# Optimization experiments

Hardware: AMD Instinct MI355X
Metric: run time of the kernel (lower is better)

Reference implementation:

```python
import jax, jax.numpy as jnp
import numpy as np

N = 100000      # nodes (single node type)
E = 400000      # edges per relation
R = 4           # relations
DIN = 128       # h_dim
H1 = 8          # heads, layer 1
DH1 = DIN // H1 # per-head dim, layer 1
DOUT = 128      # out_dim (layer 2 has 1 head of dim DOUT)
NEG_SLOPE = 0.2 # GATConv default leaky_relu slope


def gat_rel_layer(h, src, dst, W, al, ar, loop_w, bias, activation):
    """One RelationalAttLayer: per-relation GATConv (bias=False), summed across
    relations, + self-loop matmul + bias + optional relu. dropout=0.
    h: [N, din]; src/dst: [R, E]; W: [R, din, H*Dh]; al/ar: [R, H, Dh];
    loop_w: [din, dout]; bias: [dout]."""
    n = h.shape[0]

    def per_rel(src_r, dst_r, W_r, al_r, ar_r):
        nh, dh = al_r.shape
        Wh = (h @ W_r).reshape(n, nh, dh)                 # [N,H,Dh]
        el = jnp.sum(Wh * al_r, axis=-1)                  # [N,H]
        er = jnp.sum(Wh * ar_r, axis=-1)                  # [N,H]
        e = jax.nn.leaky_relu(el[src_r] + er[dst_r], NEG_SLOPE)  # [E,H]
        # edge-softmax over incoming edges per destination node (stable)
        m = jax.lax.stop_gradient(jax.ops.segment_max(e, dst_r, num_segments=n))
        ex = jnp.exp(e - m[dst_r])
        denom = jax.ops.segment_sum(ex, dst_r, num_segments=n)  # [N,H]
        alpha = ex / denom[dst_r]                                # [E,H]
        # scatter-aggregate messages
        return jax.ops.segment_sum(alpha[:, :, None] * Wh[src_r], dst_r,
                                   num_segments=n)               # [N,H,Dh]

    outs = jax.vmap(per_rel)(src, dst, W, al, ar)  # [R,N,H,Dh]
    hout = outs.sum(0).reshape(n, -1)              # cross-relation sum, flatten heads
    hout = hout + h @ loop_w + bias                # self-loop + h_bias
    if activation:
        hout = jax.nn.relu(hout)
    return hout


def setup_inputs() -> dict:
    key = jax.random.key(0)
    ks = jax.random.split(key, 14)
    s = 0.1
    return {
        "h": jax.random.normal(ks[0], (N, DIN), dtype=jnp.float32),
        "src_idx": jax.random.randint(ks[1], (R, E), 0, N, dtype=jnp.int32),
        "dst_idx": jax.random.randint(ks[2], (R, E), 0, N, dtype=jnp.int32),
        # layer 1 params (h_dim -> h_dim, H1 heads)
        "W1": jax.random.normal(ks[3], (R, DIN, H1 * DH1), dtype=jnp.float32) * s,
        "al1": jax.random.normal(ks[4], (R, H1, DH1), dtype=jnp.float32) * s,
        "ar1": jax.random.normal(ks[5], (R, H1, DH1), dtype=jnp.float32) * s,
        "loop1": jax.random.normal(ks[6], (DIN, DIN), dtype=jnp.float32) * s,
        "b1": jnp.zeros((DIN,), dtype=jnp.float32),
        # layer 2 params (h_dim -> out_dim, 1 head)
        "W2": jax.random.normal(ks[7], (R, DIN, DOUT), dtype=jnp.float32) * s,
        "al2": jax.random.normal(ks[8], (R, 1, DOUT), dtype=jnp.float32) * s,
        "ar2": jax.random.normal(ks[9], (R, 1, DOUT), dtype=jnp.float32) * s,
        "loop2": jax.random.normal(ks[10], (DIN, DOUT), dtype=jnp.float32) * s,
        "b2": jnp.zeros((DOUT,), dtype=jnp.float32),
    }


def reference(h, src_idx, dst_idx, W1, al1, ar1, loop1, b1,
              W2, al2, ar2, loop2, b2):
    # hidden layer: relu activation; last layer: no activation (last_layer_act=False)
    h1 = gat_rel_layer(h, src_idx, dst_idx, W1, al1, ar1, loop1, b1, activation=True)
    h2 = gat_rel_layer(h1, src_idx, dst_idx, W2, al2, ar2, loop2, b2, activation=False)
    return h2
```

## Files before the change

### kernel.cpp

```cpp
#include <hip/hip_runtime.h>

#define NN 100000
#define NE 400000
#define NREL 4
#define MAXDEG 24

typedef unsigned short u16;
typedef __attribute__((ext_vector_type(8))) short bf16x8;
typedef __attribute__((ext_vector_type(4))) float f32x4;

__device__ __forceinline__ u16 f2bf(float x) {
    union { float f; unsigned int u; } v; v.f = x;
    unsigned int r = v.u + 0x7fffu + ((v.u >> 16) & 1u);
    return (u16)(r >> 16);
}
__device__ __forceinline__ float bf2f(u16 x) {
    union { unsigned int u; float f; } v; v.u = ((unsigned int)x) << 16;
    return v.f;
}

__global__ __launch_bounds__(256) void zero_cnt_kernel(int* __restrict__ cnt, int n)
{
    int i = blockIdx.x * 256 + threadIdx.x;
    if (i < n) cnt[i] = 0;
}

template <bool RELU>
__global__ __launch_bounds__(256) void conv_kernel(
    const float* __restrict__ X, u16* __restrict__ Xb, int n8)
{
    int i = blockIdx.x * 256 + threadIdx.x;
    if (i >= n8) return;
    float4 a = ((const float4*)X)[2 * i];
    float4 b = ((const float4*)X)[2 * i + 1];
    if (RELU) {
        a.x = fmaxf(a.x, 0.f); a.y = fmaxf(a.y, 0.f);
        a.z = fmaxf(a.z, 0.f); a.w = fmaxf(a.w, 0.f);
        b.x = fmaxf(b.x, 0.f); b.y = fmaxf(b.y, 0.f);
        b.z = fmaxf(b.z, 0.f); b.w = fmaxf(b.w, 0.f);
    }
    ushort4 lo, hi;
    lo.x = f2bf(a.x); lo.y = f2bf(a.y); lo.z = f2bf(a.z); lo.w = f2bf(a.w);
    hi.x = f2bf(b.x); hi.y = f2bf(b.y); hi.z = f2bf(b.z); hi.w = f2bf(b.w);
    ((ushort4*)Xb)[2 * i] = lo;
    ((ushort4*)Xb)[2 * i + 1] = hi;
}

__global__ __launch_bounds__(256) void build_bcat_kernel(
    const float* __restrict__ W, const float* __restrict__ loopw,
    u16* __restrict__ Bcat)
{
    int id = blockIdx.x * 256 + threadIdx.x;
    if (id >= 5 * 16384) return;
    int slot = id >> 14, rem = id & 16383;
    int c = rem >> 7, k = rem & 127;
    const float* M = (slot < 4) ? (W + slot * 16384) : loopw;
    Bcat[(size_t)c * 640 + slot * 128 + k] = f2bf(M[k * 128 + c]);
}

__global__ __launch_bounds__(256) void build_w_kernel(
    const float* __restrict__ W, const float* __restrict__ al,
    const float* __restrict__ ar, u16* __restrict__ wcatB, int nh, int dh)
{
    int id = blockIdx.x * 256 + threadIdx.x;
    if (id >= 16384) return;
    int j = id >> 7, k = id & 127;
    int P2 = 8 * nh;
    float s = 0.f;
    if (j < P2) {
        int half = 4 * nh;
        int jj = (j < half) ? j : j - half;
        const float* av = (j < half) ? al : ar;
        int r = jj / nh, hh = jj % nh;
        for (int i = 0; i < dh; ++i)
            s += W[r * 16384 + k * 128 + hh * dh + i] * av[(r * nh + hh) * dh + i];
    }
    wcatB[j * 128 + k] = f2bf(s);
}

__global__ __launch_bounds__(256) void csr_build_kernel(
    const int* __restrict__ src, const int* __restrict__ dst,
    int* __restrict__ cur, int* __restrict__ bucket)
{
    int i = blockIdx.x * 256 + threadIdx.x;
    if (i >= NE) return;
    int d0 = dst[i],          s0 = src[i];
    int d1 = dst[NE + i],     s1 = src[NE + i];
    int d2 = dst[2 * NE + i], s2 = src[2 * NE + i];
    int d3 = dst[3 * NE + i], s3 = src[3 * NE + i];
    int p0 = atomicAdd(&cur[d0], 1);
    int p1 = atomicAdd(&cur[NN + d1], 1);
    int p2 = atomicAdd(&cur[2 * NN + d2], 1);
    int p3 = atomicAdd(&cur[3 * NN + d3], 1);
    if (p0 < MAXDEG) bucket[(size_t)d0 * MAXDEG + p0] = s0;
    if (p1 < MAXDEG) bucket[((size_t)NN + d1) * MAXDEG + p1] = s1;
    if (p2 < MAXDEG) bucket[((size_t)2 * NN + d2) * MAXDEG + p2] = s2;
    if (p3 < MAXDEG) bucket[((size_t)3 * NN + d3) * MAXDEG + p3] = s3;
}

__global__ __launch_bounds__(256) void fused_gemm_kernel(
    const u16* __restrict__ Xb, const u16* __restrict__ Bcat,
    const u16* __restrict__ wcatB, u16* __restrict__ Wh,
    float* __restrict__ O, const float* __restrict__ bias,
    float* __restrict__ elrR, int n)
{
    __shared__ u16 sA[64][136];
    __shared__ u16 sB[128][136];
    const int tid = threadIdx.x;
    const int y = blockIdx.y;
    const int row0 = blockIdx.x * 64;
    const u16* bbase; int bstride;
    if (y < 5) { bbase = Bcat + y * 128; bstride = 640; }
    else       { bbase = wcatB;          bstride = 128; }

#pragma unroll
    for (int i = 0; i < 8; ++i) {
        int idx = tid + 256 * i;
        int r = idx >> 4, ch = idx & 15;
        *(float4*)&sB[r][ch * 8] = *(const float4*)(bbase + (size_t)r * bstride + ch * 8);
    }
#pragma unroll
    for (int i = 0; i < 4; ++i) {
        int idx = tid + 256 * i;
        int r = idx >> 4, ch = idx & 15;
        int gr = row0 + r;
        float4 v = make_float4(0.f, 0.f, 0.f, 0.f);
        if (gr < n) v = *(const float4*)(Xb + (size_t)gr * 128 + ch * 8);
        *(float4*)&sA[r][ch * 8] = v;
    }
    __syncthreads();

    const int w = tid >> 6, lane = tid & 63;
    const int lr = lane & 15, hi = lane >> 4;
    f32x4 acc[8];
#pragma unroll
    for (int fn = 0; fn < 8; ++fn) acc[fn] = (f32x4){0.f, 0.f, 0.f, 0.f};
#pragma unroll
    for (int ko = 0; ko < 4; ++ko) {
        const int kk = ko * 32 + hi * 8;
        bf16x8 a = *(const bf16x8*)&sA[w * 16 + lr][kk];
#pragma unroll
        for (int fn = 0; fn < 8; ++fn) {
            bf16x8 b = *(const bf16x8*)&sB[fn * 16 + lr][kk];
            acc[fn] = __builtin_amdgcn_mfma_f32_16x16x32_bf16(a, b, acc[fn], 0, 0, 0);
        }
    }

    if (y < 4) {
        u16* Wr = Wh + (size_t)y * NN * 128;
#pragma unroll
        for (int reg = 0; reg < 4; ++reg) {
            int grow = row0 + w * 16 + hi * 4 + reg;
            if (grow >= n) continue;
            u16* crow = Wr + (size_t)grow * 128;
#pragma unroll
            for (int fn = 0; fn < 8; ++fn)
                crow[fn * 16 + lr] = f2bf(acc[fn][reg]);
        }
    } else if (y == 4) {
#pragma unroll
        for (int reg = 0; reg < 4; ++reg) {
            int grow = row0 + w * 16 + hi * 4 + reg;
            if (grow >= n) continue;
            float* crow = O + (size_t)grow * 128;
#pragma unroll
            for (int fn = 0; fn < 8; ++fn) {
                int col = fn * 16 + lr;
                crow[col] = acc[fn][reg] + bias[col];
            }
        }
    } else {
#pragma unroll
        for (int reg = 0; reg < 4; ++reg) {
            int grow = row0 + w * 16 + hi * 4 + reg;
            if (grow >= n) continue;
#pragma unroll
            for (int fn = 0; fn < 8; ++fn) {
                int col = fn * 16 + lr;
                if (col < 64) {
                    int jj  = (col < 32) ? col : col - 32;
                    int r   = jj >> 3, hh = jj & 7;
                    int off = (col < 32) ? hh : 8 + hh;
                    elrR[((size_t)r * NN + grow) * 16 + off] = acc[fn][reg];
                }
            }
        }
    }
}

__global__ __launch_bounds__(256) void elr2_gemm_kernel(
    const u16* __restrict__ Xb, const u16* __restrict__ wcatB,
    float* __restrict__ elrR, int n)
{
    __shared__ u16 sA[64][136];
    __shared__ u16 sB[16][136];
    const int tid = threadIdx.x;
    const int row0 = blockIdx.x * 64;

    if (tid < 256) {
        int r = tid >> 4, ch = tid & 15;
        *(float4*)&sB[r][ch * 8] = *(const float4*)(wcatB + (size_t)r * 128 + ch * 8);
    }
#pragma unroll
    for (int i = 0; i < 4; ++i) {
        int idx = tid + 256 * i;
        int r = idx >> 4, ch = idx & 15;
        int gr = row0 + r;
        float4 v = make_float4(0.f, 0.f, 0.f, 0.f);
        if (gr < n) v = *(const float4*)(Xb + (size_t)gr * 128 + ch * 8);
        *(float4*)&sA[r][ch * 8] = v;
    }
    __syncthreads();

    const int w = tid >> 6, lane = tid & 63;
    const int lr = lane & 15, hi = lane >> 4;
    f32x4 acc = (f32x4){0.f, 0.f, 0.f, 0.f};
#pragma unroll
    for (int ko = 0; ko < 4; ++ko) {
        const int kk = ko * 32 + hi * 8;
        bf16x8 a = *(const bf16x8*)&sA[w * 16 + lr][kk];
        bf16x8 b = *(const bf16x8*)&sB[lr][kk];
        acc = __builtin_amdgcn_mfma_f32_16x16x32_bf16(a, b, acc, 0, 0, 0);
    }
#pragma unroll
    for (int reg = 0; reg < 4; ++reg) {
        int grow = row0 + w * 16 + hi * 4 + reg;
        if (grow >= n) continue;
        int col = lr;
        if (col < 8) {
            int r = (col < 4) ? col : col - 4;
            int off = (col < 4) ? 0 : 1;
            elrR[((size_t)r * NN + grow) * 2 + off] = acc[reg];
        }
    }
}

__global__ __launch_bounds__(256) void gather_rel_kernel(
    const int* __restrict__ cnt, const int* __restrict__ bucket,
    const float* __restrict__ elP, const u16* __restrict__ WhR,
    float* __restrict__ O)
{
    const int d = blockIdx.x * 4 + (threadIdx.x >> 6);
    if (d >= NN) return;
    const int lane = threadIdx.x & 63;
    const int c0 = lane * 2;
    const int hh = c0 >> 4;

    int deg = cnt[d];
    deg = deg < 0 ? 0 : (deg > MAXDEG ? MAXDEG : deg);
    const int* bk = bucket + (size_t)d * MAXDEG;
    int4 q0 = make_int4(0, 0, 0, 0), q1 = make_int4(0, 0, 0, 0);
    if (deg > 0) q0 = *(const int4*)bk;
    if (deg > 4) q1 = *(const int4*)(bk + 4);
    const float erd = elP[(size_t)d * 16 + 8 + hh];

    float dn = 0.f, m0 = 0.f, m1 = 0.f;
    const int ss[8] = {q0.x, q0.y, q0.z, q0.w, q1.x, q1.y, q1.z, q1.w};
#pragma unroll
    for (int e = 0; e < 8; ++e) {
        int s = ss[e];
        s = ((unsigned)s < (unsigned)NN) ? s : 0;
        float v = elP[(size_t)s * 16 + hh] + erd;
        ushort2 wv = *(const ushort2*)(WhR + (size_t)s * 128 + c0);
        v = v > 0.f ? v : 0.2f * v;
        float ex = (e < deg) ? __expf(v) : 0.f;
        dn += ex;
        m0 = fmaf(ex, bf2f(wv.x), m0);
        m1 = fmaf(ex, bf2f(wv.y), m1);
    }
    for (int e = 8; e < deg; ++e) {
        int s = bk[e];
        s = ((unsigned)s < (unsigned)NN) ? s : 0;
        float v = elP[(size_t)s * 16 + hh] + erd;
        v = v > 0.f ? v : 0.2f * v;
        float ex = __expf(v);
        ushort2 wv = *(const ushort2*)(WhR + (size_t)s * 128 + c0);
        dn += ex;
        m0 = fmaf(ex, bf2f(wv.x), m0);
        m1 = fmaf(ex, bf2f(wv.y), m1);
    }
    float inv = (deg > 0) ? 1.f / dn : 0.f;
    float2* op = (float2*)(O + (size_t)d * 128) + lane;
    float2 c = *op;
    c.x += m0 * inv;
    c.y += m1 * inv;
    *op = c;
}

__global__ __launch_bounds__(256) void gather_x_kernel(
    const int* __restrict__ cnt, const int* __restrict__ bucket,
    const float* __restrict__ elrR, const u16* __restrict__ Xb,
    u16* __restrict__ Xagg)
{
    const int d = blockIdx.x;
    const int w = threadIdx.x >> 6;
    const int lane = threadIdx.x & 63;
    const int c0 = lane * 2;

    int deg = cnt[w * NN + d];
    deg = deg < 0 ? 0 : (deg > MAXDEG ? MAXDEG : deg);
    const int* bk = bucket + ((size_t)w * NN + d) * MAXDEG;
    int4 q0 = make_int4(0, 0, 0, 0), q1 = make_int4(0, 0, 0, 0);
    if (deg > 0) q0 = *(const int4*)bk;
    if (deg > 4) q1 = *(const int4*)(bk + 4);
    const float* elP = elrR + (size_t)w * NN * 2;
    const float erd = elP[(size_t)d * 2 + 1];

    float dn = 0.f, m0 = 0.f, m1 = 0.f;
    const int ss[8] = {q0.x, q0.y, q0.z, q0.w, q1.x, q1.y, q1.z, q1.w};
#pragma unroll
    for (int e = 0; e < 8; ++e) {
        int s = ss[e];
        s = ((unsigned)s < (unsigned)NN) ? s : 0;
        float v = elP[(size_t)s * 2] + erd;
        ushort2 wv = *(const ushort2*)(Xb + (size_t)s * 128 + c0);
        v = v > 0.f ? v : 0.2f * v;
        float ex = (e < deg) ? __expf(v) : 0.f;
        dn += ex;
        m0 = fmaf(ex, bf2f(wv.x), m0);
        m1 = fmaf(ex, bf2f(wv.y), m1);
    }
    for (int e = 8; e < deg; ++e) {
        int s = bk[e];
        s = ((unsigned)s < (unsigned)NN) ? s : 0;
        float v = elP[(size_t)s * 2] + erd;
        v = v > 0.f ? v : 0.2f * v;
        float ex = __expf(v);
        ushort2 wv = *(const ushort2*)(Xb + (size_t)s * 128 + c0);
        dn += ex;
        m0 = fmaf(ex, bf2f(wv.x), m0);
        m1 = fmaf(ex, bf2f(wv.y), m1);
    }
    float inv = (deg > 0) ? 1.f / dn : 0.f;
    u16* orow = Xagg + ((size_t)w * NN + d) * 128;
    ushort2 o;
    o.x = f2bf(m0 * inv);
    o.y = f2bf(m1 * inv);
    *(ushort2*)(orow + c0) = o;
}

__global__ __launch_bounds__(256) void big_gemm_kernel(
    const u16* __restrict__ Xagg, const u16* __restrict__ Xb,
    const u16* __restrict__ Bcat, const float* __restrict__ bias,
    float* __restrict__ out, int n)
{
    __shared__ u16 sA[64][136];
    __shared__ u16 sB[128][136];
    const int tid = threadIdx.x;
    const int row0 = blockIdx.x * 64;
    const int w = tid >> 6, lane = tid & 63;
    const int lr = lane & 15, hi = lane >> 4;

    f32x4 acc[8];
#pragma unroll
    for (int fn = 0; fn < 8; ++fn) acc[fn] = (f32x4){0.f, 0.f, 0.f, 0.f};

    for (int kc = 0; kc < 5; ++kc) {
        const u16* Amat = (kc < 4) ? (Xagg + (size_t)kc * NN * 128) : Xb;
        if (kc) __syncthreads();
#pragma unroll
        for (int i = 0; i < 8; ++i) {
            int idx = tid + 256 * i;
            int r = idx >> 4, ch = idx & 15;
            *(float4*)&sB[r][ch * 8] =
                *(const float4*)(Bcat + (size_t)r * 640 + kc * 128 + ch * 8);
        }
#pragma unroll
        for (int i = 0; i < 4; ++i) {
            int idx = tid + 256 * i;
            int r = idx >> 4, ch = idx & 15;
            int gr = row0 + r;
            float4 v = make_float4(0.f, 0.f, 0.f, 0.f);
            if (gr < n) v = *(const float4*)(Amat + (size_t)gr * 128 + ch * 8);
            *(float4*)&sA[r][ch * 8] = v;
        }
        __syncthreads();
#pragma unroll
        for (int ko = 0; ko < 4; ++ko) {
            const int kk = ko * 32 + hi * 8;
            bf16x8 a = *(const bf16x8*)&sA[w * 16 + lr][kk];
#pragma unroll
            for (int fn = 0; fn < 8; ++fn) {
                bf16x8 b = *(const bf16x8*)&sB[fn * 16 + lr][kk];
                acc[fn] = __builtin_amdgcn_mfma_f32_16x16x32_bf16(a, b, acc[fn], 0, 0, 0);
            }
        }
    }

#pragma unroll
    for (int reg = 0; reg < 4; ++reg) {
        int grow = row0 + w * 16 + hi * 4 + reg;
        if (grow >= n) continue;
        float* crow = out + (size_t)grow * 128;
#pragma unroll
        for (int fn = 0; fn < 8; ++fn) {
            int col = fn * 16 + lr;
            crow[col] = acc[fn][reg] + bias[col];
        }
    }
}

extern "C" void kernel_launch(void* const* d_in, const int* in_sizes, int n_in,
                              void* d_out, int out_size, void* d_ws, size_t ws_size,
                              hipStream_t stream)
{
    const float* h   = (const float*)d_in[0];
    const int*   src = (const int*)d_in[1];
    const int*   dst = (const int*)d_in[2];
    const float* W1  = (const float*)d_in[3];
    const float* al1 = (const float*)d_in[4];
    const float* ar1 = (const float*)d_in[5];
    const float* lp1 = (const float*)d_in[6];
    const float* b1  = (const float*)d_in[7];
    const float* W2  = (const float*)d_in[8];
    const float* al2 = (const float*)d_in[9];
    const float* ar2 = (const float*)d_in[10];
    const float* lp2 = (const float*)d_in[11];
    const float* b2  = (const float*)d_in[12];

    float* out = (float*)d_out;
    char*  p   = (char*)d_ws;

    const size_t szXb   = (size_t)NN * 128 * 2;
    const size_t szO    = (size_t)NN * 128 * 4;
    const size_t szElr  = (size_t)NREL * NN * 16 * 4;
    const size_t szCnt  = (size_t)NREL * NN * 4;
    const size_t szBkt  = (size_t)NREL * NN * MAXDEG * 4;
    const size_t szBcat = 5 * 16384 * 2;
    const size_t szWc   = 16384 * 2;

    u16*   Xb     = (u16*)p;    p += szXb;
    float* O1     = (float*)p;  p += szO;
    float* elrR   = (float*)p;  p += szElr;
    int*   cnt    = (int*)p;    p += szCnt;
    int*   bucket = (int*)p;    p += szBkt;
    u16*   Bcat   = (u16*)p;    p += szBcat;
    u16*   wcatB  = (u16*)p;    p += szWc;
    u16*   Wh     = (u16*)p;

    const int gg = (NN + 63) / 64;
    const int n8 = NN * 128 / 8;

    zero_cnt_kernel<<<(NREL * NN + 255) / 256, 256, 0, stream>>>(cnt, NREL * NN);
    csr_build_kernel<<<(NE + 255) / 256, 256, 0, stream>>>(src, dst, cnt, bucket);
    conv_kernel<false><<<(n8 + 255) / 256, 256, 0, stream>>>(h, Xb, n8);

    build_bcat_kernel<<<(5 * 16384) / 256, 256, 0, stream>>>(W1, lp1, Bcat);
    build_w_kernel<<<16384 / 256, 256, 0, stream>>>(W1, al1, ar1, wcatB, 8, 16);
    fused_gemm_kernel<<<dim3(gg, 6), 256, 0, stream>>>(
        Xb, Bcat, wcatB, Wh, O1, b1, elrR, NN);
    for (int r = 0; r < NREL; ++r)
        gather_rel_kernel<<<(NN + 3) / 4, 256, 0, stream>>>(
            cnt + (size_t)r * NN, bucket + (size_t)r * NN * MAXDEG,
            elrR + (size_t)r * NN * 16, Wh + (size_t)r * NN * 128, O1);
    conv_kernel<true><<<(n8 + 255) / 256, 256, 0, stream>>>(O1, Xb, n8);

    build_bcat_kernel<<<(5 * 16384) / 256, 256, 0, stream>>>(W2, lp2, Bcat);
    build_w_kernel<<<16384 / 256, 256, 0, stream>>>(W2, al2, ar2, wcatB, 1, 128);
    elr2_gemm_kernel<<<gg, 256, 0, stream>>>(Xb, wcatB, elrR, NN);
    gather_x_kernel<<<NN, 256, 0, stream>>>(cnt, bucket, elrR, Xb, Wh);
    big_gemm_kernel<<<gg, 256, 0, stream>>>(Wh, Xb, Bcat, b2, out, NN);
}
```

Measured before the change: 789.7 us.

## Fuse layer-1 relation gathers with ReLU/bf16 conversion; enlarge GEMM row tiles

```diff
diff --git a/kernel.cpp b/kernel.cpp
--- a/kernel.cpp
+++ b/kernel.cpp
@@ -25,7 +25,6 @@
     if (i < n) cnt[i] = 0;
 }
 
-template <bool RELU>
 __global__ __launch_bounds__(256) void conv_kernel(
     const float* __restrict__ X, u16* __restrict__ Xb, int n8)
 {
@@ -33,12 +32,6 @@
     if (i >= n8) return;
     float4 a = ((const float4*)X)[2 * i];
     float4 b = ((const float4*)X)[2 * i + 1];
-    if (RELU) {
-        a.x = fmaxf(a.x, 0.f); a.y = fmaxf(a.y, 0.f);
-        a.z = fmaxf(a.z, 0.f); a.w = fmaxf(a.w, 0.f);
-        b.x = fmaxf(b.x, 0.f); b.y = fmaxf(b.y, 0.f);
-        b.z = fmaxf(b.z, 0.f); b.w = fmaxf(b.w, 0.f);
-    }
     ushort4 lo, hi;
     lo.x = f2bf(a.x); lo.y = f2bf(a.y); lo.z = f2bf(a.z); lo.w = f2bf(a.w);
     hi.x = f2bf(b.x); hi.y = f2bf(b.y); hi.z = f2bf(b.z); hi.w = f2bf(b.w);
@@ -104,11 +97,11 @@
     float* __restrict__ O, const float* __restrict__ bias,
     float* __restrict__ elrR, int n)
 {
-    __shared__ u16 sA[64][136];
+    __shared__ u16 sA[128][136];
     __shared__ u16 sB[128][136];
     const int tid = threadIdx.x;
     const int y = blockIdx.y;
-    const int row0 = blockIdx.x * 64;
+    const int row0 = blockIdx.x * 128;
     const u16* bbase; int bstride;
     if (y < 5) { bbase = Bcat + y * 128; bstride = 640; }
     else       { bbase = wcatB;          bstride = 128; }
@@ -120,7 +113,7 @@
         *(float4*)&sB[r][ch * 8] = *(const float4*)(bbase + (size_t)r * bstride + ch * 8);
     }
 #pragma unroll
-    for (int i = 0; i < 4; ++i) {
+    for (int i = 0; i < 8; ++i) {
         int idx = tid + 256 * i;
         int r = idx >> 4, ch = idx & 15;
         int gr = row0 + r;
@@ -132,47 +125,58 @@
 
     const int w = tid >> 6, lane = tid & 63;
     const int lr = lane & 15, hi = lane >> 4;
-    f32x4 acc[8];
-#pragma unroll
-    for (int fn = 0; fn < 8; ++fn) acc[fn] = (f32x4){0.f, 0.f, 0.f, 0.f};
+    f32x4 acc[2][8];
+#pragma unroll
+    for (int rf = 0; rf < 2; ++rf)
+#pragma unroll
+        for (int fn = 0; fn < 8; ++fn) acc[rf][fn] = (f32x4){0.f, 0.f, 0.f, 0.f};
+
 #pragma unroll
     for (int ko = 0; ko < 4; ++ko) {
         const int kk = ko * 32 + hi * 8;
-        bf16x8 a = *(const bf16x8*)&sA[w * 16 + lr][kk];
+        bf16x8 a0 = *(const bf16x8*)&sA[w * 32 + lr][kk];
+        bf16x8 a1 = *(const bf16x8*)&sA[w * 32 + 16 + lr][kk];
 #pragma unroll
         for (int fn = 0; fn < 8; ++fn) {
             bf16x8 b = *(const bf16x8*)&sB[fn * 16 + lr][kk];
-            acc[fn] = __builtin_amdgcn_mfma_f32_16x16x32_bf16(a, b, acc[fn], 0, 0, 0);
+            acc[0][fn] = __builtin_amdgcn_mfma_f32_16x16x32_bf16(a0, b, acc[0][fn], 0, 0, 0);
+            acc[1][fn] = __builtin_amdgcn_mfma_f32_16x16x32_bf16(a1, b, acc[1][fn], 0, 0, 0);
         }
     }
 
     if (y < 4) {
         u16* Wr = Wh + (size_t)y * NN * 128;
 #pragma unroll
+        for (int rf = 0; rf < 2; ++rf)
+#pragma unroll
         for (int reg = 0; reg < 4; ++reg) {
-            int grow = row0 + w * 16 + hi * 4 + reg;
+            int grow = row0 + w * 32 + rf * 16 + hi * 4 + reg;
             if (grow >= n) continue;
             u16* crow = Wr + (size_t)grow * 128;
 #pragma unroll
             for (int fn = 0; fn < 8; ++fn)
-                crow[fn * 16 + lr] = f2bf(acc[fn][reg]);
+                crow[fn * 16 + lr] = f2bf(acc[rf][fn][reg]);
         }
     } else if (y == 4) {
 #pragma unroll
+        for (int rf = 0; rf < 2; ++rf)
+#pragma unroll
         for (int reg = 0; reg < 4; ++reg) {
-            int grow = row0 + w * 16 + hi * 4 + reg;
+            int grow = row0 + w * 32 + rf * 16 + hi * 4 + reg;
             if (grow >= n) continue;
             float* crow = O + (size_t)grow * 128;
 #pragma unroll
             for (int fn = 0; fn < 8; ++fn) {
                 int col = fn * 16 + lr;
-                crow[col] = acc[fn][reg] + bias[col];
+                crow[col] = acc[rf][fn][reg] + bias[col];
             }
         }
     } else {
 #pragma unroll
+        for (int rf = 0; rf < 2; ++rf)
+#pragma unroll
         for (int reg = 0; reg < 4; ++reg) {
-            int grow = row0 + w * 16 + hi * 4 + reg;
+            int grow = row0 + w * 32 + rf * 16 + hi * 4 + reg;
             if (grow >= n) continue;
 #pragma unroll
             for (int fn = 0; fn < 8; ++fn) {
@@ -181,7 +185,7 @@
                     int jj  = (col < 32) ? col : col - 32;
                     int r   = jj >> 3, hh = jj & 7;
                     int off = (col < 32) ? hh : 8 + hh;
-                    elrR[((size_t)r * NN + grow) * 16 + off] = acc[fn][reg];
+                    elrR[((size_t)r * NN + grow) * 16 + off] = acc[rf][fn][reg];
                 }
             }
         }
@@ -235,56 +239,82 @@
     }
 }
 
-__global__ __launch_bounds__(256) void gather_rel_kernel(
+__global__ __launch_bounds__(256) void gather_l1_kernel(
     const int* __restrict__ cnt, const int* __restrict__ bucket,
-    const float* __restrict__ elP, const u16* __restrict__ WhR,
-    float* __restrict__ O)
-{
-    const int d = blockIdx.x * 4 + (threadIdx.x >> 6);
-    if (d >= NN) return;
+    const float* __restrict__ elrR, const u16* __restrict__ Wh,
+    const float* __restrict__ Oloop, u16* __restrict__ Xb)
+{
+    const int d = blockIdx.x;
+    const int w = threadIdx.x >> 6;
     const int lane = threadIdx.x & 63;
     const int c0 = lane * 2;
     const int hh = c0 >> 4;
-
-    int deg = cnt[d];
+    __shared__ float2 part[4][64];
+
+    int deg = cnt[w * NN + d];
     deg = deg < 0 ? 0 : (deg > MAXDEG ? MAXDEG : deg);
-    const int* bk = bucket + (size_t)d * MAXDEG;
-    int4 q0 = make_int4(0, 0, 0, 0), q1 = make_int4(0, 0, 0, 0);
-    if (deg > 0) q0 = *(const int4*)bk;
-    if (deg > 4) q1 = *(const int4*)(bk + 4);
+    const int* bk = bucket + ((size_t)w * NN + d) * MAXDEG;
+    const float* elP = elrR + (size_t)w * NN * 16;
     const float erd = elP[(size_t)d * 16 + 8 + hh];
+    const u16* whr = Wh + (size_t)w * NN * 128;
 
     float dn = 0.f, m0 = 0.f, m1 = 0.f;
-    const int ss[8] = {q0.x, q0.y, q0.z, q0.w, q1.x, q1.y, q1.z, q1.w};
-#pragma unroll
-    for (int e = 0; e < 8; ++e) {
-        int s = ss[e];
-        s = ((unsigned)s < (unsigned)NN) ? s : 0;
-        float v = elP[(size_t)s * 16 + hh] + erd;
-        ushort2 wv = *(const ushort2*)(WhR + (size_t)s * 128 + c0);
-        v = v > 0.f ? v : 0.2f * v;
-        float ex = (e < deg) ? __expf(v) : 0.f;
-        dn += ex;
-        m0 = fmaf(ex, bf2f(wv.x), m0);
-        m1 = fmaf(ex, bf2f(wv.y), m1);
-    }
-    for (int e = 8; e < deg; ++e) {
-        int s = bk[e];
-        s = ((unsigned)s < (unsigned)NN) ? s : 0;
-        float v = elP[(size_t)s * 16 + hh] + erd;
-        v = v > 0.f ? v : 0.2f * v;
-        float ex = __expf(v);
-        ushort2 wv = *(const ushort2*)(WhR + (size_t)s * 128 + c0);
-        dn += ex;
-        m0 = fmaf(ex, bf2f(wv.x), m0);
-        m1 = fmaf(ex, bf2f(wv.y), m1);
+    if (deg > 0) {
+        int4 q0 = *(const int4*)bk;
+        const int ss0[4] = {q0.x, q0.y, q0.z, q0.w};
+#pragma unroll
+        for (int e = 0; e < 4; ++e) {
+            int s = ss0[e];
+            s = ((unsigned)s < (unsigned)NN) ? s : 0;
+            float v = elP[(size_t)s * 16 + hh] + erd;
+            ushort2 wv = *(const ushort2*)(whr + (size_t)s * 128 + c0);
+            v = v > 0.f ? v : 0.2f * v;
+            float ex = (e < deg) ? __expf(v) : 0.f;
+            dn += ex;
+            m0 = fmaf(ex, bf2f(wv.x), m0);
+            m1 = fmaf(ex, bf2f(wv.y), m1);
+        }
+        if (deg > 4) {
+            int4 q1 = *(const int4*)(bk + 4);
+            const int ss1[4] = {q1.x, q1.y, q1.z, q1.w};
+#pragma unroll
+            for (int e = 0; e < 4; ++e) {
+                int s = ss1[e];
+                s = ((unsigned)s < (unsigned)NN) ? s : 0;
+                float v = elP[(size_t)s * 16 + hh] + erd;
+                ushort2 wv = *(const ushort2*)(whr + (size_t)s * 128 + c0);
+                v = v > 0.f ? v : 0.2f * v;
+                float ex = (e + 4 < deg) ? __expf(v) : 0.f;
+                dn += ex;
+                m0 = fmaf(ex, bf2f(wv.x), m0);
+                m1 = fmaf(ex, bf2f(wv.y), m1);
+            }
+            for (int e = 8; e < deg; ++e) {
+                int s = bk[e];
+                s = ((unsigned)s < (unsigned)NN) ? s : 0;
+                float v = elP[(size_t)s * 16 + hh] + erd;
+                v = v > 0.f ? v : 0.2f * v;
+                float ex = __expf(v);
+                ushort2 wv = *(const ushort2*)(whr + (size_t)s * 128 + c0);
+                dn += ex;
+                m0 = fmaf(ex, bf2f(wv.x), m0);
+                m1 = fmaf(ex, bf2f(wv.y), m1);
+            }
+        }
     }
     float inv = (deg > 0) ? 1.f / dn : 0.f;
-    float2* op = (float2*)(O + (size_t)d * 128) + lane;
-    float2 c = *op;
-    c.x += m0 * inv;
-    c.y += m1 * inv;
-    *op = c;
+    part[w][lane] = make_float2(m0 * inv, m1 * inv);
+    __syncthreads();
+    if (w == 0) {
+        float2 a = part[0][lane], b = part[1][lane];
+        float2 c = part[2][lane], e4 = part[3][lane];
+        float2 ov = *((const float2*)(Oloop + (size_t)d * 128) + lane);
+        float r0 = fmaxf(ov.x + a.x + b.x + c.x + e4.x, 0.f);
+        float r1 = fmaxf(ov.y + a.y + b.y + c.y + e4.y, 0.f);
+        ushort2 o;
+        o.x = f2bf(r0); o.y = f2bf(r1);
+        *(ushort2*)(Xb + (size_t)d * 128 + c0) = o;
+    }
 }
 
 __global__ __launch_bounds__(256) void gather_x_kernel(
@@ -300,36 +330,52 @@
     int deg = cnt[w * NN + d];
     deg = deg < 0 ? 0 : (deg > MAXDEG ? MAXDEG : deg);
     const int* bk = bucket + ((size_t)w * NN + d) * MAXDEG;
-    int4 q0 = make_int4(0, 0, 0, 0), q1 = make_int4(0, 0, 0, 0);
-    if (deg > 0) q0 = *(const int4*)bk;
-    if (deg > 4) q1 = *(const int4*)(bk + 4);
     const float* elP = elrR + (size_t)w * NN * 2;
     const float erd = elP[(size_t)d * 2 + 1];
 
     float dn = 0.f, m0 = 0.f, m1 = 0.f;
-    const int ss[8] = {q0.x, q0.y, q0.z, q0.w, q1.x, q1.y, q1.z, q1.w};
-#pragma unroll
-    for (int e = 0; e < 8; ++e) {
-        int s = ss[e];
-        s = ((unsigned)s < (unsigned)NN) ? s : 0;
-        float v = elP[(size_t)s * 2] + erd;
-        ushort2 wv = *(const ushort2*)(Xb + (size_t)s * 128 + c0);
-        v = v > 0.f ? v : 0.2f * v;
-        float ex = (e < deg) ? __expf(v) : 0.f;
-        dn += ex;
-        m0 = fmaf(ex, bf2f(wv.x), m0);
-        m1 = fmaf(ex, bf2f(wv.y), m1);
-    }
-    for (int e = 8; e < deg; ++e) {
-        int s = bk[e];
-        s = ((unsigned)s < (unsigned)NN) ? s : 0;
-        float v = elP[(size_t)s * 2] + erd;
-        v = v > 0.f ? v : 0.2f * v;
-        float ex = __expf(v);
-        ushort2 wv = *(const ushort2*)(Xb + (size_t)s * 128 + c0);
-        dn += ex;
-        m0 = fmaf(ex, bf2f(wv.x), m0);
-        m1 = fmaf(ex, bf2f(wv.y), m1);
+    if (deg > 0) {
+        int4 q0 = *(const int4*)bk;
+        const int ss0[4] = {q0.x, q0.y, q0.z, q0.w};
+#pragma unroll
+        for (int e = 0; e < 4; ++e) {
+            int s = ss0[e];
+            s = ((unsigned)s < (unsigned)NN) ? s : 0;
+            float v = elP[(size_t)s * 2] + erd;
+            ushort2 wv = *(const ushort2*)(Xb + (size_t)s * 128 + c0);
+            v = v > 0.f ? v : 0.2f * v;
+            float ex = (e < deg) ? __expf(v) : 0.f;
+            dn += ex;
+            m0 = fmaf(ex, bf2f(wv.x), m0);
+            m1 = fmaf(ex, bf2f(wv.y), m1);
+        }
+        if (deg > 4) {
+            int4 q1 = *(const int4*)(bk + 4);
+            const int ss1[4] = {q1.x, q1.y, q1.z, q1.w};
+#pragma unroll
+            for (int e = 0; e < 4; ++e) {
+                int s = ss1[e];
+                s = ((unsigned)s < (unsigned)NN) ? s : 0;
+                float v = elP[(size_t)s * 2] + erd;
+                ushort2 wv = *(const ushort2*)(Xb + (size_t)s * 128 + c0);
+                v = v > 0.f ? v : 0.2f * v;
+                float ex = (e + 4 < deg) ? __expf(v) : 0.f;
+                dn += ex;
+                m0 = fmaf(ex, bf2f(wv.x), m0);
+                m1 = fmaf(ex, bf2f(wv.y), m1);
+            }
+            for (int e = 8; e < deg; ++e) {
+                int s = bk[e];
+                s = ((unsigned)s < (unsigned)NN) ? s : 0;
+                float v = elP[(size_t)s * 2] + erd;
+                v = v > 0.f ? v : 0.2f * v;
+                float ex = __expf(v);
+                ushort2 wv = *(const ushort2*)(Xb + (size_t)s * 128 + c0);
+                dn += ex;
+                m0 = fmaf(ex, bf2f(wv.x), m0);
+                m1 = fmaf(ex, bf2f(wv.y), m1);
+            }
+        }
     }
     float inv = (deg > 0) ? 1.f / dn : 0.f;
     u16* orow = Xagg + ((size_t)w * NN + d) * 128;
@@ -344,16 +390,18 @@
     const u16* __restrict__ Bcat, const float* __restrict__ bias,
     float* __restrict__ out, int n)
 {
-    __shared__ u16 sA[64][136];
+    __shared__ u16 sA[128][136];
     __shared__ u16 sB[128][136];
     const int tid = threadIdx.x;
-    const int row0 = blockIdx.x * 64;
+    const int row0 = blockIdx.x * 128;
     const int w = tid >> 6, lane = tid & 63;
     const int lr = lane & 15, hi = lane >> 4;
 
-    f32x4 acc[8];
-#pragma unroll
-    for (int fn = 0; fn < 8; ++fn) acc[fn] = (f32x4){0.f, 0.f, 0.f, 0.f};
+    f32x4 acc[2][8];
+#pragma unroll
+    for (int rf = 0; rf < 2; ++rf)
+#pragma unroll
+        for (int fn = 0; fn < 8; ++fn) acc[rf][fn] = (f32x4){0.f, 0.f, 0.f, 0.f};
 
     for (int kc = 0; kc < 5; ++kc) {
         const u16* Amat = (kc < 4) ? (Xagg + (size_t)kc * NN * 128) : Xb;
@@ -366,7 +414,7 @@
                 *(const float4*)(Bcat + (size_t)r * 640 + kc * 128 + ch * 8);
         }
 #pragma unroll
-        for (int i = 0; i < 4; ++i) {
+        for (int i = 0; i < 8; ++i) {
             int idx = tid + 256 * i;
             int r = idx >> 4, ch = idx & 15;
             int gr = row0 + r;
@@ -378,24 +426,28 @@
 #pragma unroll
         for (int ko = 0; ko < 4; ++ko) {
             const int kk = ko * 32 + hi * 8;
-            bf16x8 a = *(const bf16x8*)&sA[w * 16 + lr][kk];
+            bf16x8 a0 = *(const bf16x8*)&sA[w * 32 + lr][kk];
+            bf16x8 a1 = *(const bf16x8*)&sA[w * 32 + 16 + lr][kk];
 #pragma unroll
             for (int fn = 0; fn < 8; ++fn) {
                 bf16x8 b = *(const bf16x8*)&sB[fn * 16 + lr][kk];
-                acc[fn] = __builtin_amdgcn_mfma_f32_16x16x32_bf16(a, b, acc[fn], 0, 0, 0);
-            }
-        }
-    }
-
+                acc[0][fn] = __builtin_amdgcn_mfma_f32_16x16x32_bf16(a0, b, acc[0][fn], 0, 0, 0);
+                acc[1][fn] = __builtin_amdgcn_mfma_f32_16x16x32_bf16(a1, b, acc[1][fn], 0, 0, 0);
+            }
+        }
+    }
+
+#pragma unroll
+    for (int rf = 0; rf < 2; ++rf)
 #pragma unroll
     for (int reg = 0; reg < 4; ++reg) {
-        int grow = row0 + w * 16 + hi * 4 + reg;
+        int grow = row0 + w * 32 + rf * 16 + hi * 4 + reg;
         if (grow >= n) continue;
         float* crow = out + (size_t)grow * 128;
 #pragma unroll
         for (int fn = 0; fn < 8; ++fn) {
             int col = fn * 16 + lr;
-            crow[col] = acc[fn][reg] + bias[col];
+            crow[col] = acc[rf][fn][reg] + bias[col];
         }
     }
 }
@@ -438,26 +490,23 @@
     u16*   wcatB  = (u16*)p;    p += szWc;
     u16*   Wh     = (u16*)p;
 
-    const int gg = (NN + 63) / 64;
+    const int gg128 = (NN + 127) / 128;
+    const int gg64  = (NN + 63) / 64;
     const int n8 = NN * 128 / 8;
 
     zero_cnt_kernel<<<(NREL * NN + 255) / 256, 256, 0, stream>>>(cnt, NREL * NN);
     csr_build_kernel<<<(NE + 255) / 256, 256, 0, stream>>>(src, dst, cnt, bucket);
-    conv_kernel<false><<<(n8 + 255) / 256, 256, 0, stream>>>(h, Xb, n8);
+    conv_kernel<<<(n8 + 255) / 256, 256, 0, stream>>>(h, Xb, n8);
 
     build_bcat_kernel<<<(5 * 16384) / 256, 256, 0, stream>>>(W1, lp1, Bcat);
     build_w_kernel<<<16384 / 256, 256, 0, stream>>>(W1, al1, ar1, wcatB, 8, 16);
-    fused_gemm_kernel<<<dim3(gg, 6), 256, 0, stream>>>(
+    fused_gemm_kernel<<<dim3(gg128, 6), 256, 0, stream>>>(
         Xb, Bcat, wcatB, Wh, O1, b1, elrR, NN);
-    for (int r = 0; r < NREL; ++r)
-        gather_rel_kernel<<<(NN + 3) / 4, 256, 0, stream>>>(
-            cnt + (size_t)r * NN, bucket + (size_t)r * NN * MAXDEG,
-            elrR + (size_t)r * NN * 16, Wh + (size_t)r * NN * 128, O1);
-    conv_kernel<true><<<(n8 + 255) / 256, 256, 0, stream>>>(O1, Xb, n8);
+    gather_l1_kernel<<<NN, 256, 0, stream>>>(cnt, bucket, elrR, Wh, O1, Xb);
 
     build_bcat_kernel<<<(5 * 16384) / 256, 256, 0, stream>>>(W2, lp2, Bcat);
     build_w_kernel<<<16384 / 256, 256, 0, stream>>>(W2, al2, ar2, wcatB, 1, 128);
-    elr2_gemm_kernel<<<gg, 256, 0, stream>>>(Xb, wcatB, elrR, NN);
+    elr2_gemm_kernel<<<gg64, 256, 0, stream>>>(Xb, wcatB, elrR, NN);
     gather_x_kernel<<<NN, 256, 0, stream>>>(cnt, bucket, elrR, Xb, Wh);
-    big_gemm_kernel<<<gg, 256, 0, stream>>>(Wh, Xb, Bcat, b2, out, NN);
-}
+    big_gemm_kernel<<<gg128, 256, 0, stream>>>(Wh, Xb, Bcat, b2, out, NN);
+}
```

Result: faster. 747.9 us (-5.3%).
